# Optimization experiments

Hardware: AMD Instinct MI355X
Metric: run time of the kernel (lower is better)

## Reference

```python
import jax, jax.numpy as jnp
import numpy as np

B, T, J = 64, 1024, 22
PARENTS = [0, 0, 1, 2, 3, 0, 5, 6, 7, 0, 9, 10, 11, 12, 11, 14, 15, 16, 11, 18, 19, 20]
SPARSE_JOINTS = [0, 4, 8, 13, 17, 21]
EE = tuple(SPARSE_JOINTS[1:])                       # end effectors (sparse_joints[1:])
NO_SPARSE = tuple(j for j in range(J) if j not in SPARSE_JOINTS)
LAMBDA_EE, LAMBDA_EE_REG = 1.0, 0.1
IDENT_DQ = np.array([1, 0, 0, 0, 0, 0, 0, 0], dtype=np.float32)


def _qconj(q):
    return q * jnp.array([1.0, -1.0, -1.0, -1.0], q.dtype)


def _qmul(a, b):
    aw, ax, ay, az = a[..., 0], a[..., 1], a[..., 2], a[..., 3]
    bw, bx, by, bz = b[..., 0], b[..., 1], b[..., 2], b[..., 3]
    return jnp.stack([
        aw * bw - ax * bx - ay * by - az * bz,
        aw * bx + ax * bw + ay * bz - az * by,
        aw * by - ax * bz + ay * bw + az * bx,
        aw * bz + ax * by - ay * bx + az * bw], axis=-1)


def _qrot(q, v):
    # rotate vector v by unit quaternion q
    qv = q[..., 1:]
    t = 2.0 * jnp.cross(qv, v)
    return v + q[..., :1] * t + jnp.cross(qv, t)


def _qmat(q):
    w, x, y, z = q[..., 0], q[..., 1], q[..., 2], q[..., 3]
    m = jnp.stack([
        1 - 2 * (y * y + z * z), 2 * (x * y - w * z), 2 * (x * z + w * y),
        2 * (x * y + w * z), 1 - 2 * (x * x + z * z), 2 * (y * z - w * x),
        2 * (x * z - w * y), 2 * (y * z + w * x), 1 - 2 * (x * x + y * y)], axis=-1)
    return m.reshape(m.shape[:-1] + (3, 3))


def _denorm_to_dq(x, mean, std, set_root_identity):
    # x: (B, J*8, T) channel-major dual quats -> (B, T, J, 8)
    x = x * std[None, :, None] + mean[None, :, None]
    if set_root_identity:
        x = x.at[:, :8, :].set(jnp.asarray(IDENT_DQ, x.dtype)[None, :, None])
    b, c, t = x.shape
    return x.reshape(b, c // 8, 8, t).transpose(0, 3, 1, 2)


def _local_rot_from_dq(dq):
    # skeleton_from_dual_quat: real part = global rotation; make local via parent gather
    qr = dq[..., :4]
    qr = qr / jnp.linalg.norm(qr, axis=-1, keepdims=True)
    parent = jnp.asarray(PARENTS)
    local = _qmul(_qconj(qr[:, :, parent, :]), qr)   # (B,T,J,4)
    # forward_ik overwrites root local rotation with identity
    local = local.at[:, :, 0, :].set(jnp.array([1.0, 0.0, 0.0, 0.0], dq.dtype))
    return local


def _fk(local_rot, offsets):
    # fk_2: sequential parent-indexed propagation; root global pos is zeros
    rots = [local_rot[:, :, 0]]
    poss = [jnp.zeros(local_rot.shape[:2] + (3,), local_rot.dtype)]
    for j in range(1, J):
        p = PARENTS[j]
        rots.append(_qmul(rots[p], local_rot[:, :, j]))
        poss.append(_qrot(rots[p], offsets[j]) + poss[p])
    grot = jnp.stack(rots, axis=2)          # (B,T,J,4)
    pos = jnp.stack(poss, axis=2)           # (B,T,J,3)
    return pos, _qmat(grot)                  # positions, (B,T,J,3,3) rot matrices


def setup_inputs() -> dict:
    key = jax.random.key(0)
    ks = jax.random.split(key, 7)
    C = J * 8
    return {
        "input": jax.random.normal(ks[0], (B, C, T), jnp.float32),
        "input_ik": jax.random.normal(ks[1], (B, C - 8, T), jnp.float32),
        "input_decoder": jax.random.normal(ks[2], (B, C, T), jnp.float32),
        "target": jax.random.normal(ks[3], (B, C, T), jnp.float32),
        "mean_dqs": 0.1 * jax.random.normal(ks[4], (C,), jnp.float32),
        "std_dqs": 0.5 + 0.5 * jax.random.uniform(ks[5], (C,), jnp.float32),
        "offsets": jax.random.normal(ks[6], (J, 3), jnp.float32),
    }


def reference(input, input_ik, input_decoder, target, mean_dqs, std_dqs, offsets):
    # prepend identity-slot for the root (8 zero channels), then denormalize
    dq_ik = jnp.concatenate([jnp.zeros_like(input_ik[:, :8, :]), input_ik], axis=1)
    dq_ik = _denorm_to_dq(dq_ik, mean_dqs, std_dqs, True)
    dq_dec = _denorm_to_dq(input_decoder, mean_dqs, std_dqs, True)
    dq_tgt = _denorm_to_dq(target, mean_dqs, std_dqs, False)

    r_ik = _local_rot_from_dq(dq_ik)
    r_dec = _local_rot_from_dq(dq_dec)
    r_tgt = _local_rot_from_dq(dq_tgt)

    pos, rm = _fk(r_ik, offsets)
    tpos, trm = _fk(r_tgt, offsets)
    dpos, drm = _fk(r_dec, offsets)

    ee = jnp.asarray(EE)
    ns = jnp.asarray(NO_SPARSE)
    mse = lambda a, b: jnp.mean((a - b) ** 2)
    loss_ee = mse(pos[:, :, ee], tpos[:, :, ee]) + mse(rm[:, :, ee], trm[:, :, ee])
    loss_reg = mse(dpos[:, :, ns], pos[:, :, ns]) + mse(drm[:, :, ns], rm[:, :, ns])
    return loss_ee * LAMBDA_EE + loss_reg * LAMBDA_EE_REG
```

## Files before the change

kernel.cpp:

```cpp
#include <hip/hip_runtime.h>


#define T_DIM 1024

struct alignas(8) F2 { float u, v; };

__device__ __forceinline__ F2 operator+(F2 a, F2 b){ return {a.u+b.u, a.v+b.v}; }
__device__ __forceinline__ F2 operator-(F2 a, F2 b){ return {a.u-b.u, a.v-b.v}; }
__device__ __forceinline__ F2 operator*(F2 a, F2 b){ return {a.u*b.u, a.v*b.v}; }
__device__ __forceinline__ F2 operator*(F2 a, float s){ return {a.u*s, a.v*s}; }
__device__ __forceinline__ F2 operator+(F2 a, float s){ return {a.u+s, a.v+s}; }
__device__ __forceinline__ F2 f2neg(F2 a){ return {-a.u, -a.v}; }
__device__ __forceinline__ F2 f2bc(float s){ return {s, s}; }
__device__ __forceinline__ F2 f2rsq(F2 a){ return {rsqrtf(a.u), rsqrtf(a.v)}; }

struct Q2 { F2 w, x, y, z; };
struct V2 { F2 x, y, z; };
struct St2 { Q2 rot; V2 pos; };

__device__ __forceinline__ Q2 qmul2(const Q2 a, const Q2 b) {
    Q2 r;
    r.w = a.w*b.w - a.x*b.x - a.y*b.y - a.z*b.z;
    r.x = a.w*b.x + a.x*b.w + a.y*b.z - a.z*b.y;
    r.y = a.w*b.y - a.x*b.z + a.y*b.w + a.z*b.x;
    r.z = a.w*b.z + a.x*b.y - a.y*b.x + a.z*b.w;
    return r;
}

__device__ __forceinline__ V2 qrot2(const Q2 q, float ox, float oy, float oz) {
    F2 tx = (q.y*oz - q.z*oy)*2.f;
    F2 ty = (q.z*ox - q.x*oz)*2.f;
    F2 tz = (q.x*oy - q.y*ox)*2.f;
    V2 r;
    r.x = (q.w*tx + (q.y*tz - q.z*ty)) + ox;
    r.y = (q.w*ty + (q.z*tx - q.x*tz)) + oy;
    r.z = (q.w*tz + (q.x*ty - q.y*tx)) + oz;
    return r;
}

__device__ __forceinline__ F2 rmdiff2u(const Q2 a, const Q2 b) {
    F2 d = a.w*b.w + a.x*b.x + a.y*b.y + a.z*b.z;
    return (f2bc(1.f) - d*d)*8.f;
}

__device__ __forceinline__ F2 pdiff2(const V2 a, const V2 b) {
    F2 dx = a.x-b.x, dy = a.y-b.y, dz = a.z-b.z;
    return dx*dx + dy*dy + dz*dz;
}

__device__ __forceinline__ Q2 mkq2(const F2 r[4], const int c0,
                                   const float* __restrict__ mean,
                                   const float* __restrict__ stdv) {
    Q2 q;
    q.w = r[0]*stdv[c0+0] + mean[c0+0];
    q.x = r[1]*stdv[c0+1] + mean[c0+1];
    q.y = r[2]*stdv[c0+2] + mean[c0+2];
    q.z = r[3]*stdv[c0+3] + mean[c0+3];
    F2 inv = f2rsq(q.w*q.w + q.x*q.x + q.y*q.y + q.z*q.z);
    q.w = q.w*inv; q.x = q.x*inv; q.y = q.y*inv; q.z = q.z*inv;
    return q;
}

__device__ __forceinline__ F2 ld2(const float* __restrict__ base, int idx) {
    return *reinterpret_cast<const F2*>(base + idx);
}

template<int J0>
__device__ __forceinline__ void ldb3(
    const float* __restrict__ xp, const float* __restrict__ yp, const int t0,
    F2 (*X)[4], F2 (*Y)[4])
{
#pragma unroll
    for (int jj = 0; jj < 3; ++jj) {
#pragma unroll
        for (int c = 0; c < 4; ++c) {
            X[jj][c] = ld2(xp, ((J0+jj)*8 + c)*T_DIM + t0);
            Y[jj][c] = ld2(yp, ((J0+jj)*8 + c)*T_DIM + t0);
        }
    }
}

template<int J, bool LOSS, bool PRE>
__device__ __forceinline__ void stepf(
    St2& sx, St2& sy,
    const F2 xr[4], const F2 yr[4],
    const float* __restrict__ mean, const float* __restrict__ stdv,
    const float* __restrict__ offs, const Q2& q0c,
    F2& ap, F2& ar)
{
    const int c0 = J*8;
    Q2 qx = mkq2(xr, c0, mean, stdv);
    Q2 qy = mkq2(yr, c0, mean, stdv);
    if (PRE) qy = qmul2(q0c, qy);
    const float ox = offs[3*J], oy = offs[3*J+1], oz = offs[3*J+2];
    V2 dx = qrot2(sx.rot, ox, oy, oz);
    V2 dy = qrot2(sy.rot, ox, oy, oz);
    V2 px = { dx.x + sx.pos.x, dx.y + sx.pos.y, dx.z + sx.pos.z };
    V2 py = { dy.x + sy.pos.x, dy.y + sy.pos.y, dy.z + sy.pos.z };
    if (LOSS) {
        ap = ap + pdiff2(px, py);
        ar = ar + rmdiff2u(qx, qy);
    }
    sx.rot = qx; sx.pos = px;
    sy.rot = qy; sy.pos = py;
}

template<bool EEROLE>
__device__ __forceinline__ void walk(
    const float* __restrict__ xp, const float* __restrict__ yp, const int t0,
    const float* __restrict__ mean, const float* __restrict__ stdv,
    const float* __restrict__ offs, F2& ap, F2& ar)
{
    F2 Ax[3][4], Ay[3][4], Bx[3][4], By[3][4];
    F2 rq0[4];

    if (EEROLE) {
#pragma unroll
        for (int c = 0; c < 4; ++c) rq0[c] = ld2(yp, c*T_DIM + t0);
    }
    ldb3<1>(xp, yp, t0, Ax, Ay);
    ldb3<4>(xp, yp, t0, Bx, By);

    Q2 q0c = { f2bc(1.f), f2bc(0.f), f2bc(0.f), f2bc(0.f) };
    if (EEROLE) {
        Q2 q0 = mkq2(rq0, 0, mean, stdv);
        q0c = { q0.w, f2neg(q0.x), f2neg(q0.y), f2neg(q0.z) };
    }
    const St2 root = { { f2bc(1.f), f2bc(0.f), f2bc(0.f), f2bc(0.f) },
                       { f2bc(0.f), f2bc(0.f), f2bc(0.f) } };
    St2 sx = root, sy = root;
    St2 sx11, sy11;

    stepf<1, !EEROLE, EEROLE>(sx,sy, Ax[0],Ay[0], mean,stdv,offs,q0c, ap,ar);
    stepf<2, !EEROLE, EEROLE>(sx,sy, Ax[1],Ay[1], mean,stdv,offs,q0c, ap,ar);
    stepf<3, !EEROLE, EEROLE>(sx,sy, Ax[2],Ay[2], mean,stdv,offs,q0c, ap,ar);
    ldb3<7>(xp, yp, t0, Ax, Ay);

    stepf<4,  EEROLE, EEROLE>(sx,sy, Bx[0],By[0], mean,stdv,offs,q0c, ap,ar);
    sx = root; sy = root;
    stepf<5, !EEROLE, EEROLE>(sx,sy, Bx[1],By[1], mean,stdv,offs,q0c, ap,ar);
    stepf<6, !EEROLE, EEROLE>(sx,sy, Bx[2],By[2], mean,stdv,offs,q0c, ap,ar);
    ldb3<10>(xp, yp, t0, Bx, By);

    stepf<7, !EEROLE, EEROLE>(sx,sy, Ax[0],Ay[0], mean,stdv,offs,q0c, ap,ar);
    stepf<8,  EEROLE, EEROLE>(sx,sy, Ax[1],Ay[1], mean,stdv,offs,q0c, ap,ar);
    sx = root; sy = root;
    stepf<9, !EEROLE, EEROLE>(sx,sy, Ax[2],Ay[2], mean,stdv,offs,q0c, ap,ar);
    ldb3<13>(xp, yp, t0, Ax, Ay);

    stepf<10, !EEROLE, EEROLE>(sx,sy, Bx[0],By[0], mean,stdv,offs,q0c, ap,ar);
    stepf<11, !EEROLE, EEROLE>(sx,sy, Bx[1],By[1], mean,stdv,offs,q0c, ap,ar);
    sx11 = sx; sy11 = sy;
    stepf<12, !EEROLE, EEROLE>(sx,sy, Bx[2],By[2], mean,stdv,offs,q0c, ap,ar);
    ldb3<16>(xp, yp, t0, Bx, By);

    stepf<13,  EEROLE, EEROLE>(sx,sy, Ax[0],Ay[0], mean,stdv,offs,q0c, ap,ar);
    sx = sx11; sy = sy11;
    stepf<14, !EEROLE, EEROLE>(sx,sy, Ax[1],Ay[1], mean,stdv,offs,q0c, ap,ar);
    stepf<15, !EEROLE, EEROLE>(sx,sy, Ax[2],Ay[2], mean,stdv,offs,q0c, ap,ar);
    ldb3<19>(xp, yp, t0, Ax, Ay);

    stepf<16, !EEROLE, EEROLE>(sx,sy, Bx[0],By[0], mean,stdv,offs,q0c, ap,ar);
    stepf<17,  EEROLE, EEROLE>(sx,sy, Bx[1],By[1], mean,stdv,offs,q0c, ap,ar);
    sx = sx11; sy = sy11;
    stepf<18, !EEROLE, EEROLE>(sx,sy, Bx[2],By[2], mean,stdv,offs,q0c, ap,ar);

    stepf<19, !EEROLE, EEROLE>(sx,sy, Ax[0],Ay[0], mean,stdv,offs,q0c, ap,ar);
    stepf<20, !EEROLE, EEROLE>(sx,sy, Ax[1],Ay[1], mean,stdv,offs,q0c, ap,ar);
    stepf<21,  EEROLE, EEROLE>(sx,sy, Ax[2],Ay[2], mean,stdv,offs,q0c, ap,ar);
}

__global__ __launch_bounds__(256) void fk_loss_kernel(
    const float* __restrict__ ik, const float* __restrict__ dec,
    const float* __restrict__ tgt, const float* __restrict__ mean,
    const float* __restrict__ stdv, const float* __restrict__ offs,
    float* __restrict__ out)
{
    __shared__ float swred[4];
    const int tid = threadIdx.x;
    const int bid = blockIdx.x;
    const int role = bid >> 7;
    const int pb   = bid & 127;
    const int bb   = pb >> 1;
    const int t0   = (pb & 1)*512 + 2*tid;

    const float* ikp = ik  + (size_t)bb * (168*1024) - (size_t)(8*T_DIM);
    const float* dep = dec + (size_t)bb * (176*1024);
    const float* tgp = tgt + (size_t)bb * (176*1024);

    F2 ap = f2bc(0.f), ar = f2bc(0.f);
    float loss;
    const float BT = 65536.f;
    if (role == 0) {
        walk<true>(ikp, tgp, t0, mean, stdv, offs, ap, ar);
        loss = (ap.u + ap.v) * (1.0f/(BT*15.f))
             + (ar.u + ar.v) * (1.0f/(BT*45.f));
    } else {
        walk<false>(dep, ikp, t0, mean, stdv, offs, ap, ar);
        loss = (ap.u + ap.v) * (0.1f/(BT*48.f))
             + (ar.u + ar.v) * (0.1f/(BT*144.f));
    }

#pragma unroll
    for (int o = 32; o > 0; o >>= 1) loss += __shfl_down(loss, o);
    if ((tid & 63) == 0) swred[tid >> 6] = loss;
    __syncthreads();
    if (tid == 0) {
        atomicAdd(out, swred[0]+swred[1]+swred[2]+swred[3]);
    }
}

extern "C" void kernel_launch(void* const* d_in, const int* in_sizes, int n_in,
                              void* d_out, int out_size, void* d_ws, size_t ws_size,
                              hipStream_t stream) {
    const float* ikx  = (const float*)d_in[1];
    const float* dec  = (const float*)d_in[2];
    const float* tgt  = (const float*)d_in[3];
    const float* mean = (const float*)d_in[4];
    const float* stdv = (const float*)d_in[5];
    const float* offs = (const float*)d_in[6];
    float* out = (float*)d_out;

    hipMemsetAsync(out, 0, sizeof(float), stream);
    fk_loss_kernel<<<256, 256, 0, stream>>>(ikx, dec, tgt, mean, stdv, offs, out);
}
```

Baseline: 184.3 us.

## Stage joint inputs into LDS via async global_load_lds double buffering

Replaces the per-thread register prefetch of joint channels with asynchronous global-to-LDS DMA loads into two 32KB LDS buffers. Each pair of joints is staged by all four waves, with vmcnt waits and block barriers gating consumption. The aim is to overlap memory latency with FK compute and to free registers. In exchange it adds a barrier at every stage and uses 64KB of dynamic LDS, which limits blocks per CU. The final reduction scratch now reuses the LDS buffer.

```diff
diff --git a/kernel.cpp b/kernel.cpp
--- a/kernel.cpp
+++ b/kernel.cpp
@@ -2,6 +2,19 @@
 
 
 #define T_DIM 1024
+#define SB() __builtin_amdgcn_sched_barrier(0)
+
+#define GATE(N) do { SB(); \
+    asm volatile("s_waitcnt vmcnt(" #N ")" ::: "memory"); SB(); \
+    __builtin_amdgcn_s_barrier(); } while (0)
+#define ENDB() do { SB(); __builtin_amdgcn_s_barrier(); } while (0)
+
+typedef __attribute__((address_space(1))) const float glb_cf;
+typedef __attribute__((address_space(3))) float lds_f;
+
+__device__ __forceinline__ void dma16(const float* g, float* l) {
+    __builtin_amdgcn_global_load_lds((glb_cf*)g, (lds_f*)l, 16, 0, 0);
+}
 
 struct alignas(8) F2 { float u, v; };
 
@@ -61,33 +74,42 @@
     return q;
 }
 
-__device__ __forceinline__ F2 ld2(const float* __restrict__ base, int idx) {
-    return *reinterpret_cast<const F2*>(base + idx);
-}
-
-template<int J0>
-__device__ __forceinline__ void ldb3(
-    const float* __restrict__ xp, const float* __restrict__ yp, const int t0,
-    F2 (*X)[4], F2 (*Y)[4])
-{
-#pragma unroll
-    for (int jj = 0; jj < 3; ++jj) {
-#pragma unroll
-        for (int c = 0; c < 4; ++c) {
-            X[jj][c] = ld2(xp, ((J0+jj)*8 + c)*T_DIM + t0);
-            Y[jj][c] = ld2(yp, ((J0+jj)*8 + c)*T_DIM + t0);
-        }
+template<int J0, int NJ>
+__device__ __forceinline__ void stage(
+    const float* __restrict__ xp, const float* __restrict__ yp,
+    float* __restrict__ lbuf, const int tblk, const int w, const int lane)
+{
+    constexpr int per = NJ*16/4;
+#pragma unroll
+    for (int q = 0; q < per; ++q) {
+        const int k  = w*per + q;
+        const int r  = k >> 1;
+        const int h  = k & 1;
+        const int jj = r >> 3;
+        const int s  = (r >> 2) & 1;
+        const int ch = r & 3;
+        const float* sb = s ? yp : xp;
+        const float* g = sb + ((J0+jj)*8 + ch)*T_DIM + tblk + h*256 + lane*4;
+        float* l = lbuf + r*512 + h*256;
+        dma16(g, l);
     }
 }
 
 template<int J, bool LOSS, bool PRE>
-__device__ __forceinline__ void stepf(
-    St2& sx, St2& sy,
-    const F2 xr[4], const F2 yr[4],
+__device__ __forceinline__ void stepl(
+    St2& sx, St2& sy, const float* __restrict__ lds, const int t0,
     const float* __restrict__ mean, const float* __restrict__ stdv,
-    const float* __restrict__ offs, const Q2& q0c,
-    F2& ap, F2& ar)
-{
+    const float* __restrict__ offs, const Q2& q0c, F2& ap, F2& ar)
+{
+    constexpr int c  = (J-1) >> 1;
+    constexpr int jj = (J-1) & 1;
+    constexpr int fb = (c & 1)*8192 + jj*8*512;
+    F2 xr[4], yr[4];
+#pragma unroll
+    for (int ch = 0; ch < 4; ++ch) {
+        xr[ch] = *reinterpret_cast<const F2*>(lds + fb + ch*512 + t0);
+        yr[ch] = *reinterpret_cast<const F2*>(lds + fb + (4+ch)*512 + t0);
+    }
     const int c0 = J*8;
     Q2 qx = mkq2(xr, c0, mean, stdv);
     Q2 qy = mkq2(yr, c0, mean, stdv);
@@ -105,21 +127,34 @@
     sy.rot = qy; sy.pos = py;
 }
 
+constexpr bool kEE[22] = {false,false,false,false,true,  false,false,false,true,
+                          false,false,false,false,true,  false,false,false,true,
+                          false,false,false,true};
+
+#define STEPJ(J) stepl<J, (EEROLE ? kEE[J] : !kEE[J]), EEROLE>( \
+                     sx, sy, lds, t0, mean, stdv, offs, q0c, ap, ar)
+
 template<bool EEROLE>
-__device__ __forceinline__ void walk(
-    const float* __restrict__ xp, const float* __restrict__ yp, const int t0,
+__device__ __forceinline__ void walkL(
+    const float* __restrict__ xp, const float* __restrict__ yp,
+    float* __restrict__ lds, const int tblk, const int t0,
+    const int w, const int lane,
     const float* __restrict__ mean, const float* __restrict__ stdv,
     const float* __restrict__ offs, F2& ap, F2& ar)
 {
-    F2 Ax[3][4], Ay[3][4], Bx[3][4], By[3][4];
+    float* b0 = lds;
+    float* b1 = lds + 8192;
+
     F2 rq0[4];
-
     if (EEROLE) {
 #pragma unroll
-        for (int c = 0; c < 4; ++c) rq0[c] = ld2(yp, c*T_DIM + t0);
-    }
-    ldb3<1>(xp, yp, t0, Ax, Ay);
-    ldb3<4>(xp, yp, t0, Bx, By);
+        for (int c2 = 0; c2 < 4; ++c2)
+            rq0[c2] = *reinterpret_cast<const F2*>(yp + c2*T_DIM + tblk + t0);
+    }
+
+    stage<1,2>(xp, yp, b0, tblk, w, lane);
+    stage<3,2>(xp, yp, b1, tblk, w, lane);
+    GATE(8);
 
     Q2 q0c = { f2bc(1.f), f2bc(0.f), f2bc(0.f), f2bc(0.f) };
     if (EEROLE) {
@@ -131,43 +166,54 @@
     St2 sx = root, sy = root;
     St2 sx11, sy11;
 
-    stepf<1, !EEROLE, EEROLE>(sx,sy, Ax[0],Ay[0], mean,stdv,offs,q0c, ap,ar);
-    stepf<2, !EEROLE, EEROLE>(sx,sy, Ax[1],Ay[1], mean,stdv,offs,q0c, ap,ar);
-    stepf<3, !EEROLE, EEROLE>(sx,sy, Ax[2],Ay[2], mean,stdv,offs,q0c, ap,ar);
-    ldb3<7>(xp, yp, t0, Ax, Ay);
-
-    stepf<4,  EEROLE, EEROLE>(sx,sy, Bx[0],By[0], mean,stdv,offs,q0c, ap,ar);
+    STEPJ(1); STEPJ(2);
+    ENDB();
+    stage<5,2>(xp, yp, b0, tblk, w, lane);
+    GATE(8);
+    STEPJ(3); STEPJ(4);
+    ENDB();
+    stage<7,2>(xp, yp, b1, tblk, w, lane);
+    GATE(8);
     sx = root; sy = root;
-    stepf<5, !EEROLE, EEROLE>(sx,sy, Bx[1],By[1], mean,stdv,offs,q0c, ap,ar);
-    stepf<6, !EEROLE, EEROLE>(sx,sy, Bx[2],By[2], mean,stdv,offs,q0c, ap,ar);
-    ldb3<10>(xp, yp, t0, Bx, By);
-
-    stepf<7, !EEROLE, EEROLE>(sx,sy, Ax[0],Ay[0], mean,stdv,offs,q0c, ap,ar);
-    stepf<8,  EEROLE, EEROLE>(sx,sy, Ax[1],Ay[1], mean,stdv,offs,q0c, ap,ar);
+    STEPJ(5); STEPJ(6);
+    ENDB();
+    stage<9,2>(xp, yp, b0, tblk, w, lane);
+    GATE(8);
+    STEPJ(7); STEPJ(8);
+    ENDB();
+    stage<11,2>(xp, yp, b1, tblk, w, lane);
+    GATE(8);
     sx = root; sy = root;
-    stepf<9, !EEROLE, EEROLE>(sx,sy, Ax[2],Ay[2], mean,stdv,offs,q0c, ap,ar);
-    ldb3<13>(xp, yp, t0, Ax, Ay);
-
-    stepf<10, !EEROLE, EEROLE>(sx,sy, Bx[0],By[0], mean,stdv,offs,q0c, ap,ar);
-    stepf<11, !EEROLE, EEROLE>(sx,sy, Bx[1],By[1], mean,stdv,offs,q0c, ap,ar);
+    STEPJ(9); STEPJ(10);
+    ENDB();
+    stage<13,2>(xp, yp, b0, tblk, w, lane);
+    GATE(8);
+    STEPJ(11);
     sx11 = sx; sy11 = sy;
-    stepf<12, !EEROLE, EEROLE>(sx,sy, Bx[2],By[2], mean,stdv,offs,q0c, ap,ar);
-    ldb3<16>(xp, yp, t0, Bx, By);
-
-    stepf<13,  EEROLE, EEROLE>(sx,sy, Ax[0],Ay[0], mean,stdv,offs,q0c, ap,ar);
+    STEPJ(12);
+    ENDB();
+    stage<15,2>(xp, yp, b1, tblk, w, lane);
+    GATE(8);
+    STEPJ(13);
     sx = sx11; sy = sy11;
-    stepf<14, !EEROLE, EEROLE>(sx,sy, Ax[1],Ay[1], mean,stdv,offs,q0c, ap,ar);
-    stepf<15, !EEROLE, EEROLE>(sx,sy, Ax[2],Ay[2], mean,stdv,offs,q0c, ap,ar);
-    ldb3<19>(xp, yp, t0, Ax, Ay);
-
-    stepf<16, !EEROLE, EEROLE>(sx,sy, Bx[0],By[0], mean,stdv,offs,q0c, ap,ar);
-    stepf<17,  EEROLE, EEROLE>(sx,sy, Bx[1],By[1], mean,stdv,offs,q0c, ap,ar);
+    STEPJ(14);
+    ENDB();
+    stage<17,2>(xp, yp, b0, tblk, w, lane);
+    GATE(8);
+    STEPJ(15); STEPJ(16);
+    ENDB();
+    stage<19,2>(xp, yp, b1, tblk, w, lane);
+    GATE(8);
+    STEPJ(17);
     sx = sx11; sy = sy11;
-    stepf<18, !EEROLE, EEROLE>(sx,sy, Bx[2],By[2], mean,stdv,offs,q0c, ap,ar);
-
-    stepf<19, !EEROLE, EEROLE>(sx,sy, Ax[0],Ay[0], mean,stdv,offs,q0c, ap,ar);
-    stepf<20, !EEROLE, EEROLE>(sx,sy, Ax[1],Ay[1], mean,stdv,offs,q0c, ap,ar);
-    stepf<21,  EEROLE, EEROLE>(sx,sy, Ax[2],Ay[2], mean,stdv,offs,q0c, ap,ar);
+    STEPJ(18);
+    ENDB();
+    stage<21,1>(xp, yp, b0, tblk, w, lane);
+    GATE(4);
+    STEPJ(19); STEPJ(20);
+    ENDB();
+    GATE(0);
+    STEPJ(21);
 }
 
 __global__ __launch_bounds__(256) void fk_loss_kernel(
@@ -176,13 +222,16 @@
     const float* __restrict__ stdv, const float* __restrict__ offs,
     float* __restrict__ out)
 {
-    __shared__ float swred[4];
+    extern __shared__ float lds[];
     const int tid = threadIdx.x;
     const int bid = blockIdx.x;
     const int role = bid >> 7;
     const int pb   = bid & 127;
     const int bb   = pb >> 1;
-    const int t0   = (pb & 1)*512 + 2*tid;
+    const int tblk = (pb & 1) * 512;
+    const int t0   = 2 * tid;
+    const int w    = tid >> 6;
+    const int lane = tid & 63;
 
     const float* ikp = ik  + (size_t)bb * (168*1024) - (size_t)(8*T_DIM);
     const float* dep = dec + (size_t)bb * (176*1024);
@@ -192,17 +241,18 @@
     float loss;
     const float BT = 65536.f;
     if (role == 0) {
-        walk<true>(ikp, tgp, t0, mean, stdv, offs, ap, ar);
+        walkL<true>(ikp, tgp, lds, tblk, t0, w, lane, mean, stdv, offs, ap, ar);
         loss = (ap.u + ap.v) * (1.0f/(BT*15.f))
              + (ar.u + ar.v) * (1.0f/(BT*45.f));
     } else {
-        walk<false>(dep, ikp, t0, mean, stdv, offs, ap, ar);
+        walkL<false>(dep, ikp, lds, tblk, t0, w, lane, mean, stdv, offs, ap, ar);
         loss = (ap.u + ap.v) * (0.1f/(BT*48.f))
              + (ar.u + ar.v) * (0.1f/(BT*144.f));
     }
 
 #pragma unroll
     for (int o = 32; o > 0; o >>= 1) loss += __shfl_down(loss, o);
+    float* swred = lds + 4096;
     if ((tid & 63) == 0) swred[tid >> 6] = loss;
     __syncthreads();
     if (tid == 0) {
@@ -222,5 +272,5 @@
     float* out = (float*)d_out;
 
     hipMemsetAsync(out, 0, sizeof(float), stream);
-    fk_loss_kernel<<<256, 256, 0, stream>>>(ikx, dec, tgt, mean, stdv, offs, out);
-}
+    fk_loss_kernel<<<256, 256, 65536, stream>>>(ikx, dec, tgt, mean, stdv, offs, out);
+}
```

After: 198.9 us. 7.9% more time.
